# Optimization experiments

Measured on AMD Instinct MI355X. Metric: run time of the kernel, lower is better.

The kernel has to match this reference:

```python
import jax, jax.numpy as jnp
import numpy as np
from jax import lax

NPOINT = 1024
K = 32
EPS = 1e-5  # BatchNorm eps (eval mode, running stats)


def _fps(xyz, npoint):
    """Farthest point sampling. xyz: [B,N,3] -> idx [B,npoint] (int32).
    Deterministic start at index 0 (torch version starts at a random index)."""
    B, N, _ = xyz.shape
    barange = jnp.arange(B)

    def step(carry, _):
        distance, farthest = carry
        centroid = xyz[barange, farthest]                    # [B,3]
        d = jnp.sum((xyz - centroid[:, None, :]) ** 2, -1)   # [B,N]
        distance = jnp.minimum(distance, d)
        new_far = jnp.argmax(distance, axis=-1).astype(jnp.int32)
        return (distance, new_far), farthest

    init = (jnp.full((B, N), 1e10, dtype=xyz.dtype), jnp.zeros((B,), jnp.int32))
    _, centroids = lax.scan(step, init, None, length=npoint)  # [npoint,B]
    return centroids.T                                        # [B,npoint]


def _square_distance(src, dst):
    # src [B,M,3], dst [B,N,3] -> [B,M,N]
    return (jnp.sum(src ** 2, -1)[:, :, None]
            - 2.0 * jnp.einsum('bmc,bnc->bmn', src, dst)
            + jnp.sum(dst ** 2, -1)[:, None, :])


def _gather(p, idx):
    # p [B,N,C], idx [B,...] -> [B,...,C]
    return jax.vmap(lambda pb, ib: pb[ib])(p, idx)


def _mlp_layer(x, w, cb, g, b, m, v):
    # x [B,S,K,Cin]; Conv2d 1x1 == channel matmul, then eval-mode BN, ReLU
    x = jnp.einsum('bskc,oc->bsko', x, w) + cb
    x = (x - m) * (g / jnp.sqrt(v + EPS)) + b
    return jax.nn.relu(x)


def _forward(xyz, points, w0, cb0, g0, b0, m0, v0,
             w1, cb1, g1, b1, m1, v1, w2, cb2, g2, b2, m2, v2):
    fps_idx = _fps(xyz, NPOINT)                       # [B,S]
    new_xyz = _gather(xyz, fps_idx)                   # [B,S,3]
    dists = _square_distance(new_xyz, xyz)            # [B,S,N]
    _, nn_idx = lax.top_k(-dists, K)                  # [B,S,K]
    grouped_xyz = _gather(xyz, nn_idx)                # [B,S,K,3]
    grouped_xyz_norm = grouped_xyz - new_xyz[:, :, None, :]
    grouped_pts = _gather(points, nn_idx)             # [B,S,K,C]
    x = jnp.concatenate([grouped_xyz_norm, grouped_pts], axis=-1)  # [B,S,K,3+C]
    x = _mlp_layer(x, w0, cb0, g0, b0, m0, v0)
    x = _mlp_layer(x, w1, cb1, g1, b1, m1, v1)
    x = _mlp_layer(x, w2, cb2, g2, b2, m2, v2)
    new_points = jnp.max(x, axis=2)                   # max over K -> [B,S,Cout]
    return new_xyz, jnp.transpose(new_points, (0, 2, 1))  # [B,Cout,S]


def setup_inputs() -> dict:
    key = jax.random.key(0)
    ks = jax.random.split(key, 8)
    B, N, C = 16, 4096, 64
    inp = {
        'xyz': jax.random.normal(ks[0], (B, N, 3), jnp.float32),
        'points': jax.random.normal(ks[1], (B, N, C), jnp.float32),
    }
    channels = [(3 + C, 64), (64, 64), (64, 128)]
    for li, (ci, co) in enumerate(channels):
        inp[f'w{li}'] = jax.random.normal(ks[2 + li], (co, ci), jnp.float32) * 0.05
        inp[f'cb{li}'] = jnp.zeros((co,), jnp.float32)
        inp[f'g{li}'] = jnp.ones((co,), jnp.float32)
        inp[f'b{li}'] = jnp.zeros((co,), jnp.float32)
        inp[f'm{li}'] = jnp.zeros((co,), jnp.float32)
        inp[f'v{li}'] = jnp.ones((co,), jnp.float32)
    return inp


def reference(xyz, points, w0, cb0, g0, b0, m0, v0,
              w1, cb1, g1, b1, m1, v1, w2, cb2, g2, b2, m2, v2):
    return _forward(xyz, points, w0, cb0, g0, b0, m0, v0,
                    w1, cb1, g1, b1, m1, v1, w2, cb2, g2, b2, m2, v2)
```

## Files before the change

kernel.cpp:

```cpp
#include <hip/hip_runtime.h>
#include <math.h>

#define NPTS 4096
#define NB 16
#define NS 1024
#define KNB 32
#define CPTS 64

#define FLAG_OFF_B  0
#define CNT_OFF_B   64
#define PUBC_OFF_B  128
#define WFRAG_ELEMS 18432
#define NUNITS      16384
#define CAP         256

typedef __attribute__((ext_vector_type(8))) short short8;
typedef __attribute__((ext_vector_type(4))) float f32x4;

__device__ __forceinline__ short f2bf(float f) {
  unsigned u = __float_as_uint(f);
  unsigned r = (u + 0x7fffu + ((u >> 16) & 1u)) >> 16;
  return (short)r;
}

template <int CTRL>
__device__ __forceinline__ int dppmov(int cur) {
  return __builtin_amdgcn_update_dpp(cur, cur, CTRL, 0xF, 0xF, false);
}
template <int CTRL>
__device__ __forceinline__ void dpp_max_u64(unsigned& hi, unsigned& lo) {
  unsigned nhi = (unsigned)dppmov<CTRL>((int)hi);
  unsigned nlo = (unsigned)dppmov<CTRL>((int)lo);
  bool gt = (nhi > hi) || (nhi == hi && nlo > lo);
  hi = gt ? nhi : hi;
  lo = gt ? nlo : lo;
}
template <int CTRL>
__device__ __forceinline__ void dpp_fmax(float& m) {
  m = fmaxf(m, __int_as_float(dppmov<CTRL>(__float_as_int(m))));
}
template <int CTRL>
__device__ __forceinline__ void dpp_umin(unsigned& v) {
  unsigned o = (unsigned)dppmov<CTRL>((int)v);
  v = (o < v) ? o : v;
}

#define XSTR 104
__global__ __launch_bounds__(512, 2) void fused_kernel(
    const float* __restrict__ xyz, const float* __restrict__ points,
    const float* __restrict__ w0, const float* __restrict__ cb0, const float* __restrict__ g0,
    const float* __restrict__ b0, const float* __restrict__ m0, const float* __restrict__ v0,
    const float* __restrict__ w1, const float* __restrict__ cb1, const float* __restrict__ g1,
    const float* __restrict__ b1, const float* __restrict__ m1, const float* __restrict__ v1,
    const float* __restrict__ w2, const float* __restrict__ cb2, const float* __restrict__ g2,
    const float* __restrict__ b2, const float* __restrict__ m2, const float* __restrict__ v2,
    char* __restrict__ wsb, float* __restrict__ newxyz, float* __restrict__ outp) {
  struct FpsSh {
    float4 sxyz4[NPTS];
    float4 centL[NS];
    unsigned long long part[2][8];
  };
  struct WorkerSh {
    short Wlds[WFRAG_ELEMS];
    short X[8][32 * XSTR];
    unsigned long long cand[8][CAP];
    int nnL[8][KNB];
    float biasL[256];
    unsigned cnt[8];
  };
  __shared__ union { FpsSh f; WorkerSh w; } sh;

  const int t = threadIdx.x;
  const int lane = t & 63;
  const int wave = t >> 6;
  unsigned* flagp = (unsigned*)(wsb + FLAG_OFF_B);
  unsigned* cntp  = (unsigned*)(wsb + CNT_OFF_B);
  float* pubC = (float*)(wsb + PUBC_OFF_B);

  if (blockIdx.x < NB) {
    const int b = blockIdx.x;
    const float* xb = xyz + (size_t)b * NPTS * 3;
    float* outb = newxyz + (size_t)b * NS * 3;

    for (int i = t; i < NPTS; i += 512)
      sh.f.sxyz4[i] = make_float4(xb[i * 3 + 0], xb[i * 3 + 1], xb[i * 3 + 2], 0.f);

    float px[8], py[8], pz[8], dist[8];
#pragma unroll
    for (int j = 0; j < 8; ++j) {
      int n = t + 512 * j;
      px[j] = xb[n * 3 + 0];
      py[j] = xb[n * 3 + 1];
      pz[j] = xb[n * 3 + 2];
      dist[j] = 1e10f;
    }
    __syncthreads();
    float cx = sh.f.sxyz4[0].x, cy = sh.f.sxyz4[0].y, cz = sh.f.sxyz4[0].z;
    if (t == 0) sh.f.centL[0] = sh.f.sxyz4[0];

    for (int it = 1; it < NS; ++it) {
      const int buf = it & 1;
      float dm[8];
#pragma unroll
      for (int j = 0; j < 8; ++j) {
        float dx = __fsub_rn(px[j], cx);
        float dy = __fsub_rn(py[j], cy);
        float dz = __fsub_rn(pz[j], cz);
        float d  = __fadd_rn(__fadd_rn(__fmul_rn(dx, dx), __fmul_rn(dy, dy)), __fmul_rn(dz, dz));
        float v  = fminf(dist[j], d);
        dist[j] = v;
        dm[j] = v;
      }
      float m = fmaxf(fmaxf(fmaxf(dm[0], dm[1]), fmaxf(dm[2], dm[3])),
                      fmaxf(fmaxf(dm[4], dm[5]), fmaxf(dm[6], dm[7])));
      dpp_fmax<0xB1>(m);  dpp_fmax<0x4E>(m);  dpp_fmax<0x141>(m);
      dpp_fmax<0x140>(m); dpp_fmax<0x142>(m); dpp_fmax<0x143>(m);
      float M = __int_as_float(__builtin_amdgcn_readlane(__float_as_int(m), 63));
      unsigned idxl = 0xFFFFFFFFu;
#pragma unroll
      for (int j = 7; j >= 0; --j) idxl = (dm[j] == M) ? (unsigned)(t + 512 * j) : idxl;
      dpp_umin<0xB1>(idxl);  dpp_umin<0x4E>(idxl);  dpp_umin<0x141>(idxl);
      dpp_umin<0x140>(idxl); dpp_umin<0x142>(idxl); dpp_umin<0x143>(idxl);
      if (lane == 63)
        sh.f.part[buf][wave] = ((unsigned long long)__float_as_uint(M) << 32) | (unsigned)(~idxl);
      __syncthreads();
      unsigned long long k0 = sh.f.part[buf][lane & 7];
      unsigned khi = (unsigned)(k0 >> 32), klo = (unsigned)k0;
      dpp_max_u64<0xB1>(khi, klo);
      dpp_max_u64<0x4E>(khi, klo);
      dpp_max_u64<0x141>(khi, klo);
      int bi = (int)(~klo) & 4095;
      float4 c4 = sh.f.sxyz4[bi];
      cx = c4.x; cy = c4.y; cz = c4.z;
      if (t == 0) sh.f.centL[it] = c4;
      if ((it & 31) == 31 && wave == 0) {
        if (lane == 0)
          __hip_atomic_store(&flagp[b], (unsigned)(it - 31), __ATOMIC_RELEASE, __HIP_MEMORY_SCOPE_AGENT);
        if (lane < 32) {
          int ci = it - 31 + lane;
          float4 cc = sh.f.centL[ci];
          float* dst = pubC + ((size_t)b * NS + ci) * 3;
          __hip_atomic_store(dst + 0, cc.x, __ATOMIC_RELAXED, __HIP_MEMORY_SCOPE_AGENT);
          __hip_atomic_store(dst + 1, cc.y, __ATOMIC_RELAXED, __HIP_MEMORY_SCOPE_AGENT);
          __hip_atomic_store(dst + 2, cc.z, __ATOMIC_RELAXED, __HIP_MEMORY_SCOPE_AGENT);
        }
      }
    }
    if (wave == 0 && lane == 0)
      __hip_atomic_store(&flagp[b], (unsigned)NS, __ATOMIC_RELEASE, __HIP_MEMORY_SCOPE_AGENT);
    __syncthreads();
    const float* cf = (const float*)sh.f.centL;
    for (int i = t; i < NS * 3; i += 512) {
      int p = i / 3, c = i - p * 3;
      outb[i] = cf[p * 4 + c];
    }
  }

  __syncthreads();
  for (int i = t; i < WFRAG_ELEMS; i += 512) {
    int g = i >> 9, ln = (i >> 3) & 63, j = i & 7;
    int l, nt, s;
    if (g < 12)      { l = 0; nt = g / 3;  s = g % 3; }
    else if (g < 20) { l = 1; int gg = g - 12; nt = gg >> 1; s = gg & 1; }
    else             { l = 2; int gg = g - 20; nt = gg >> 1; s = gg & 1; }
    int n = nt * 16 + (ln & 15);
    int k = s * 32 + ((ln >> 4) << 3) + j;
    float val = 0.f;
    if (l == 0) { if (k < 67) val = w0[n * 67 + k] * (g0[n] / sqrtf(v0[n] + 1e-5f)); }
    else if (l == 1) { val = w1[n * 64 + k] * (g1[n] / sqrtf(v1[n] + 1e-5f)); }
    else { val = w2[n * 64 + k] * (g2[n] / sqrtf(v2[n] + 1e-5f)); }
    sh.w.Wlds[i] = f2bf(val);
  }
  if (t < 256) {
    int o = t;
    float bv;
    if (o < 64)       { float sc = g0[o] / sqrtf(v0[o] + 1e-5f); bv = (cb0[o] - m0[o]) * sc + b0[o]; }
    else if (o < 128) { int c = o - 64;  float sc = g1[c] / sqrtf(v1[c] + 1e-5f); bv = (cb1[c] - m1[c]) * sc + b1[c]; }
    else              { int c = o - 128; float sc = g2[c] / sqrtf(v2[c] + 1e-5f); bv = (cb2[c] - m2[c]) * sc + b2[c]; }
    sh.w.biasL[o] = bv;
  }
  __syncthreads();

  unsigned long long* cand = sh.w.cand[wave];

  for (;;) {
    unsigned u = 0;
    if (lane == 0) u = atomicAdd(cntp, 1u);
    u = (unsigned)__builtin_amdgcn_readfirstlane((int)u);
    if (u >= NUNITS) break;
    const int b = (int)(u & 15u);
    const int s = (int)(u >> 4);

    {
      unsigned need = (unsigned)s + 1u;
      while (__hip_atomic_load(&flagp[b], __ATOMIC_ACQUIRE, __HIP_MEMORY_SCOPE_AGENT) < need)
        __builtin_amdgcn_s_sleep(64);
    }
    const float* qcp = pubC + ((size_t)b * NS + s) * 3;
    float qx = __hip_atomic_load(qcp + 0, __ATOMIC_RELAXED, __HIP_MEMORY_SCOPE_AGENT);
    float qy = __hip_atomic_load(qcp + 1, __ATOMIC_RELAXED, __HIP_MEMORY_SCOPE_AGENT);
    float qz = __hip_atomic_load(qcp + 2, __ATOMIC_RELAXED, __HIP_MEMORY_SCOPE_AGENT);

    const float* xb = xyz + (size_t)b * NPTS * 3;
    float s2 = __fadd_rn(__fadd_rn(__fmul_rn(qx, qx), __fmul_rn(qy, qy)), __fmul_rn(qz, qz));

    unsigned long long mkey = 0xFFFFFFFFFFFFFFFFull;
#pragma unroll 4
    for (int j = 0; j < 64; ++j) {
      int n = j * 64 + lane;
      float px = xb[n * 3], py = xb[n * 3 + 1], pz = xb[n * 3 + 2];
      float n2 = __fadd_rn(__fadd_rn(__fmul_rn(px, px), __fmul_rn(py, py)), __fmul_rn(pz, pz));
      float dt = __fadd_rn(__fadd_rn(__fmul_rn(qx, px), __fmul_rn(qy, py)), __fmul_rn(qz, pz));
      float d  = __fadd_rn(__fsub_rn(s2, __fmul_rn(2.0f, dt)), n2);
      unsigned uu = __float_as_uint(d);
      uu ^= (0x80000000u | (unsigned)((int)uu >> 31));
      unsigned long long key = ((unsigned long long)uu << 32) | (unsigned)n;
      mkey = key < mkey ? key : mkey;
    }

    {
      unsigned mh = (unsigned)(mkey >> 32), ml2 = (unsigned)mkey;
#pragma unroll
      for (int k = 2; k <= 64; k <<= 1) {
#pragma unroll
        for (int j = k >> 1; j >= 1; j >>= 1) {
          unsigned oh = (unsigned)__shfl_xor((int)mh, j, 64);
          unsigned ol = (unsigned)__shfl_xor((int)ml2, j, 64);
          bool up = (lane & k) == 0;
          bool lower = (lane & j) == 0;
          bool omin = (oh < mh) || (oh == mh && ol < ml2);
          bool keep_o = (lower == up) ? omin : !omin;
          mh = keep_o ? oh : mh;
          ml2 = keep_o ? ol : ml2;
        }
      }
      unsigned th = (unsigned)__builtin_amdgcn_readlane((int)mh, 31);
      unsigned tl = (unsigned)__builtin_amdgcn_readlane((int)ml2, 31);
      mkey = ((unsigned long long)th << 32) | tl;
    }
    const unsigned long long tau = mkey;

    if (lane == 0) sh.w.cnt[wave] = 0;
    asm volatile("s_waitcnt lgkmcnt(0)" ::: "memory");
#pragma unroll 4
    for (int j = 0; j < 64; ++j) {
      int n = j * 64 + lane;
      float px = xb[n * 3], py = xb[n * 3 + 1], pz = xb[n * 3 + 2];
      float n2 = __fadd_rn(__fadd_rn(__fmul_rn(px, px), __fmul_rn(py, py)), __fmul_rn(pz, pz));
      float dt = __fadd_rn(__fadd_rn(__fmul_rn(qx, px), __fmul_rn(qy, py)), __fmul_rn(qz, pz));
      float d  = __fadd_rn(__fsub_rn(s2, __fmul_rn(2.0f, dt)), n2);
      unsigned uu = __float_as_uint(d);
      uu ^= (0x80000000u | (unsigned)((int)uu >> 31));
      unsigned long long key = ((unsigned long long)uu << 32) | (unsigned)n;
      if (key <= tau) {
        unsigned pos = atomicAdd(&sh.w.cnt[wave], 1u);
        if (pos < CAP) cand[pos] = key;
      }
    }
    asm volatile("s_waitcnt lgkmcnt(0)" ::: "memory");
    unsigned cn = sh.w.cnt[wave];
    if (cn > CAP) cn = CAP;

    for (unsigned base = 0; base < cn; base += 64) {
      unsigned i = base + (unsigned)lane;
      unsigned long long ki = (i < cn) ? cand[i] : 0xFFFFFFFFFFFFFFFFull;
      int rank = 0;
#pragma unroll 4
      for (unsigned c2 = 0; c2 < cn; ++c2)
        rank += (cand[c2] < ki) ? 1 : 0;
      if (i < cn && rank < KNB) sh.w.nnL[wave][rank] = (int)(unsigned)(ki & 0xFFFFFFFFull);
    }
    asm volatile("s_waitcnt lgkmcnt(0)" ::: "memory");

    {
      const int qi = wave;
      const float* pb = points + (size_t)b * NPTS * CPTS;
      const float* bias = sh.w.biasL;
      short* X = sh.w.X[qi];

      {
        int r = lane & 31, half = lane >> 5;
        int idx = sh.w.nnL[qi][r];
        const float* prow = pb + (size_t)idx * CPTS;
#pragma unroll
        for (int i = 0; i < 48; ++i) {
          int c = half * 48 + i;
          float v;
          if (c < 3) {
            float qc = (c == 0) ? qx : ((c == 1) ? qy : qz);
            v = __fsub_rn(xb[idx * 3 + c], qc);
          } else if (c < 67) {
            v = prow[c - 3];
          } else {
            v = 0.f;
          }
          X[r * XSTR + c] = f2bf(v);
        }
      }

      const int ml = lane & 15, quad = lane >> 4;
      const short8* Wf = (const short8*)sh.w.Wlds;

      short8 a0[2][3];
#pragma unroll
      for (int m2 = 0; m2 < 2; ++m2)
#pragma unroll
        for (int s3 = 0; s3 < 3; ++s3)
          a0[m2][s3] = *(const short8*)&X[(m2 * 16 + ml) * XSTR + s3 * 32 + quad * 8];
      f32x4 acc0[2][4];
#pragma unroll
      for (int m2 = 0; m2 < 2; ++m2)
#pragma unroll
        for (int nt = 0; nt < 4; ++nt) {
          f32x4 c = {0.f, 0.f, 0.f, 0.f};
#pragma unroll
          for (int s3 = 0; s3 < 3; ++s3)
            c = __builtin_amdgcn_mfma_f32_16x16x32_bf16(a0[m2][s3], Wf[(nt * 3 + s3) * 64 + lane], c, 0, 0, 0);
          acc0[m2][nt] = c;
        }
#pragma unroll
      for (int m2 = 0; m2 < 2; ++m2)
#pragma unroll
        for (int nt = 0; nt < 4; ++nt) {
          int ch = nt * 16 + ml;
          float bv = bias[ch];
#pragma unroll
          for (int r4 = 0; r4 < 4; ++r4) {
            float y = fmaxf(acc0[m2][nt][r4] + bv, 0.f);
            int m = quad * 4 + r4;
            int sK = ch >> 5, qq = (ch >> 3) & 3, jj = ch & 7;
            X[((m2 * 2 + sK) * 64 + qq * 16 + m) * 8 + jj] = f2bf(y);
          }
        }

      short8 a1[2][2];
#pragma unroll
      for (int m2 = 0; m2 < 2; ++m2)
#pragma unroll
        for (int sK = 0; sK < 2; ++sK)
          a1[m2][sK] = *(const short8*)&X[((m2 * 2 + sK) * 64 + lane) * 8];
      f32x4 acc1[2][4];
#pragma unroll
      for (int m2 = 0; m2 < 2; ++m2)
#pragma unroll
        for (int nt = 0; nt < 4; ++nt) {
          f32x4 c = {0.f, 0.f, 0.f, 0.f};
#pragma unroll
          for (int sK = 0; sK < 2; ++sK)
            c = __builtin_amdgcn_mfma_f32_16x16x32_bf16(a1[m2][sK], Wf[(12 + nt * 2 + sK) * 64 + lane], c, 0, 0, 0);
          acc1[m2][nt] = c;
        }
#pragma unroll
      for (int m2 = 0; m2 < 2; ++m2)
#pragma unroll
        for (int nt = 0; nt < 4; ++nt) {
          int ch = nt * 16 + ml;
          float bv = bias[64 + ch];
#pragma unroll
          for (int r4 = 0; r4 < 4; ++r4) {
            float y = fmaxf(acc1[m2][nt][r4] + bv, 0.f);
            int m = quad * 4 + r4;
            int sK = ch >> 5, qq = (ch >> 3) & 3, jj = ch & 7;
            X[((m2 * 2 + sK) * 64 + qq * 16 + m) * 8 + jj] = f2bf(y);
          }
        }

      short8 a2[2][2];
#pragma unroll
      for (int m2 = 0; m2 < 2; ++m2)
#pragma unroll
        for (int sK = 0; sK < 2; ++sK)
          a2[m2][sK] = *(const short8*)&X[((m2 * 2 + sK) * 64 + lane) * 8];
#pragma unroll
      for (int nt = 0; nt < 8; ++nt) {
        f32x4 c0 = {0.f, 0.f, 0.f, 0.f}, c1 = {0.f, 0.f, 0.f, 0.f};
        short8 w0f = Wf[(20 + nt * 2 + 0) * 64 + lane];
        short8 w1f = Wf[(20 + nt * 2 + 1) * 64 + lane];
        c0 = __builtin_amdgcn_mfma_f32_16x16x32_bf16(a2[0][0], w0f, c0, 0, 0, 0);
        c0 = __builtin_amdgcn_mfma_f32_16x16x32_bf16(a2[0][1], w1f, c0, 0, 0, 0);
        c1 = __builtin_amdgcn_mfma_f32_16x16x32_bf16(a2[1][0], w0f, c1, 0, 0, 0);
        c1 = __builtin_amdgcn_mfma_f32_16x16x32_bf16(a2[1][1], w1f, c1, 0, 0, 0);
        float bv = bias[128 + nt * 16 + ml];
        float m = -1.f;
#pragma unroll
        for (int r4 = 0; r4 < 4; ++r4) {
          m = fmaxf(m, fmaxf(c0[r4] + bv, 0.f));
          m = fmaxf(m, fmaxf(c1[r4] + bv, 0.f));
        }
        m = fmaxf(m, __shfl_xor(m, 16, 64));
        m = fmaxf(m, __shfl_xor(m, 32, 64));
        if (lane < 16) outp[((size_t)b * 128 + nt * 16 + lane) * NS + s] = m;
      }
    }
  }
}

extern "C" void kernel_launch(void* const* d_in, const int* in_sizes, int n_in,
                              void* d_out, int out_size, void* d_ws, size_t ws_size,
                              hipStream_t stream) {
  const float* xyz    = (const float*)d_in[0];
  const float* points = (const float*)d_in[1];
  const float* w0  = (const float*)d_in[2];
  const float* cb0 = (const float*)d_in[3];
  const float* g0  = (const float*)d_in[4];
  const float* b0  = (const float*)d_in[5];
  const float* m0  = (const float*)d_in[6];
  const float* v0  = (const float*)d_in[7];
  const float* w1  = (const float*)d_in[8];
  const float* cb1 = (const float*)d_in[9];
  const float* g1  = (const float*)d_in[10];
  const float* b1  = (const float*)d_in[11];
  const float* m1  = (const float*)d_in[12];
  const float* v1  = (const float*)d_in[13];
  const float* w2  = (const float*)d_in[14];
  const float* cb2 = (const float*)d_in[15];
  const float* g2  = (const float*)d_in[16];
  const float* b2  = (const float*)d_in[17];
  const float* m2  = (const float*)d_in[18];
  const float* v2  = (const float*)d_in[19];

  char*  wsb    = (char*)d_ws;
  float* newxyz = (float*)d_out;
  float* outp   = (float*)d_out + (size_t)NB * NS * 3;

  hipMemsetAsync(wsb, 0, 128, stream);
  fused_kernel<<<256, 512, 0, stream>>>(
      xyz, points, w0, cb0, g0, b0, m0, v0, w1, cb1, g1, b1, m1, v1,
      w2, cb2, g2, b2, m2, v2, wsb, newxyz, outp);
}
```

Measured before the change: 955.3 us.

## Batch work grabs, cache FPS flags, vectorize gather, reorder layer-0 channels

Workers now claim 8 units per atomic and keep a per-batch cache of the last seen FPS progress flag in a lane register, so they poll the global flag less often. The FPS publisher swaps its release stores for an explicit vmcnt wait plus a relaxed store, and the per-lane argmax index reduction becomes a tree instead of a serial chain. The neighbor feature gather is rewritten to use float4 loads and short8 LDS stores. To allow this, layer-0 weights are permuted so the 64 point features come first and the 3 xyz offsets sit at columns 64-66, with X zero-filled once up front. The weaker acquire semantics on the flag and pubC loads carry a memory-ordering risk.

```diff
diff --git a/kernel.cpp b/kernel.cpp
--- a/kernel.cpp
+++ b/kernel.cpp
@@ -13,6 +13,7 @@
 #define WFRAG_ELEMS 18432
 #define NUNITS      16384
 #define CAP         256
+#define GRAB        8
 
 typedef __attribute__((ext_vector_type(8))) short short8;
 typedef __attribute__((ext_vector_type(4))) float f32x4;
@@ -116,9 +117,18 @@
       dpp_fmax<0xB1>(m);  dpp_fmax<0x4E>(m);  dpp_fmax<0x141>(m);
       dpp_fmax<0x140>(m); dpp_fmax<0x142>(m); dpp_fmax<0x143>(m);
       float M = __int_as_float(__builtin_amdgcn_readlane(__float_as_int(m), 63));
-      unsigned idxl = 0xFFFFFFFFu;
-#pragma unroll
-      for (int j = 7; j >= 0; --j) idxl = (dm[j] == M) ? (unsigned)(t + 512 * j) : idxl;
+      unsigned i0 = (dm[0] == M) ? (unsigned)(t + 512 * 0) : 0xFFFFFFFFu;
+      unsigned i1 = (dm[1] == M) ? (unsigned)(t + 512 * 1) : 0xFFFFFFFFu;
+      unsigned i2 = (dm[2] == M) ? (unsigned)(t + 512 * 2) : 0xFFFFFFFFu;
+      unsigned i3 = (dm[3] == M) ? (unsigned)(t + 512 * 3) : 0xFFFFFFFFu;
+      unsigned i4 = (dm[4] == M) ? (unsigned)(t + 512 * 4) : 0xFFFFFFFFu;
+      unsigned i5 = (dm[5] == M) ? (unsigned)(t + 512 * 5) : 0xFFFFFFFFu;
+      unsigned i6 = (dm[6] == M) ? (unsigned)(t + 512 * 6) : 0xFFFFFFFFu;
+      unsigned i7 = (dm[7] == M) ? (unsigned)(t + 512 * 7) : 0xFFFFFFFFu;
+      unsigned a01 = i0 < i1 ? i0 : i1, a23 = i2 < i3 ? i2 : i3;
+      unsigned a45 = i4 < i5 ? i4 : i5, a67 = i6 < i7 ? i6 : i7;
+      unsigned a03 = a01 < a23 ? a01 : a23, a47 = a45 < a67 ? a45 : a67;
+      unsigned idxl = a03 < a47 ? a03 : a47;
       dpp_umin<0xB1>(idxl);  dpp_umin<0x4E>(idxl);  dpp_umin<0x141>(idxl);
       dpp_umin<0x140>(idxl); dpp_umin<0x142>(idxl); dpp_umin<0x143>(idxl);
       if (lane == 63)
@@ -134,8 +144,10 @@
       cx = c4.x; cy = c4.y; cz = c4.z;
       if (t == 0) sh.f.centL[it] = c4;
       if ((it & 31) == 31 && wave == 0) {
-        if (lane == 0)
-          __hip_atomic_store(&flagp[b], (unsigned)(it - 31), __ATOMIC_RELEASE, __HIP_MEMORY_SCOPE_AGENT);
+        if (lane == 0) {
+          asm volatile("s_waitcnt vmcnt(0)" ::: "memory");
+          __hip_atomic_store(&flagp[b], (unsigned)(it - 31), __ATOMIC_RELAXED, __HIP_MEMORY_SCOPE_AGENT);
+        }
         if (lane < 32) {
           int ci = it - 31 + lane;
           float4 cc = sh.f.centL[ci];
@@ -146,8 +158,10 @@
         }
       }
     }
-    if (wave == 0 && lane == 0)
-      __hip_atomic_store(&flagp[b], (unsigned)NS, __ATOMIC_RELEASE, __HIP_MEMORY_SCOPE_AGENT);
+    if (wave == 0 && lane == 0) {
+      asm volatile("s_waitcnt vmcnt(0)" ::: "memory");
+      __hip_atomic_store(&flagp[b], (unsigned)NS, __ATOMIC_RELAXED, __HIP_MEMORY_SCOPE_AGENT);
+    }
     __syncthreads();
     const float* cf = (const float*)sh.f.centL;
     for (int i = t; i < NS * 3; i += 512) {
@@ -166,7 +180,11 @@
     int n = nt * 16 + (ln & 15);
     int k = s * 32 + ((ln >> 4) << 3) + j;
     float val = 0.f;
-    if (l == 0) { if (k < 67) val = w0[n * 67 + k] * (g0[n] / sqrtf(v0[n] + 1e-5f)); }
+    if (l == 0) {
+      float sc = g0[n] / sqrtf(v0[n] + 1e-5f);
+      if (k < 64)      val = w0[n * 67 + (k + 3)] * sc;
+      else if (k < 67) val = w0[n * 67 + (k - 64)] * sc;
+    }
     else if (l == 1) { val = w1[n * 64 + k] * (g1[n] / sqrtf(v1[n] + 1e-5f)); }
     else { val = w2[n * 64 + k] * (g2[n] / sqrtf(v2[n] + 1e-5f)); }
     sh.w.Wlds[i] = f2bf(val);
@@ -182,19 +200,35 @@
   __syncthreads();
 
   unsigned long long* cand = sh.w.cand[wave];
+  for (int i = lane; i < (32 * XSTR) / 2; i += 64) ((int*)sh.w.X[wave])[i] = 0;
+
+  unsigned fcache = 0;
 
   for (;;) {
-    unsigned u = 0;
-    if (lane == 0) u = atomicAdd(cntp, 1u);
-    u = (unsigned)__builtin_amdgcn_readfirstlane((int)u);
-    if (u >= NUNITS) break;
+    unsigned base = 0;
+    if (lane == 0) base = atomicAdd(cntp, (unsigned)GRAB);
+    base = (unsigned)__builtin_amdgcn_readfirstlane((int)base);
+    if (base >= NUNITS) break;
+    unsigned uend = base + GRAB;
+    if (uend > NUNITS) uend = NUNITS;
+
+    for (unsigned u = base; u < uend; ++u) {
     const int b = (int)(u & 15u);
     const int s = (int)(u >> 4);
 
     {
       unsigned need = (unsigned)s + 1u;
-      while (__hip_atomic_load(&flagp[b], __ATOMIC_ACQUIRE, __HIP_MEMORY_SCOPE_AGENT) < need)
-        __builtin_amdgcn_s_sleep(64);
+      unsigned have = (unsigned)__shfl((int)fcache, b, 64);
+      if (have < need) {
+        unsigned f;
+        for (;;) {
+          f = __hip_atomic_load(&flagp[b], __ATOMIC_RELAXED, __HIP_MEMORY_SCOPE_AGENT);
+          if (f >= need) break;
+          __builtin_amdgcn_s_sleep(64);
+        }
+        if (lane == b) fcache = f;
+        asm volatile("" ::: "memory");
+      }
     }
     const float* qcp = pubC + ((size_t)b * NS + s) * 3;
     float qx = __hip_atomic_load(qcp + 0, __ATOMIC_RELAXED, __HIP_MEMORY_SCOPE_AGENT);
@@ -261,8 +295,8 @@
     unsigned cn = sh.w.cnt[wave];
     if (cn > CAP) cn = CAP;
 
-    for (unsigned base = 0; base < cn; base += 64) {
-      unsigned i = base + (unsigned)lane;
+    for (unsigned bb = 0; bb < cn; bb += 64) {
+      unsigned i = bb + (unsigned)lane;
       unsigned long long ki = (i < cn) ? cand[i] : 0xFFFFFFFFFFFFFFFFull;
       int rank = 0;
 #pragma unroll 4
@@ -279,23 +313,24 @@
       short* X = sh.w.X[qi];
 
       {
-        int r = lane & 31, half = lane >> 5;
+        int h = lane & 1, r = lane >> 1;
         int idx = sh.w.nnL[qi][r];
-        const float* prow = pb + (size_t)idx * CPTS;
-#pragma unroll
-        for (int i = 0; i < 48; ++i) {
-          int c = half * 48 + i;
-          float v;
-          if (c < 3) {
-            float qc = (c == 0) ? qx : ((c == 1) ? qy : qz);
-            v = __fsub_rn(xb[idx * 3 + c], qc);
-          } else if (c < 67) {
-            v = prow[c - 3];
-          } else {
-            v = 0.f;
-          }
-          X[r * XSTR + c] = f2bf(v);
-        }
+        const f32x4* src = (const f32x4*)(pb + (size_t)idx * CPTS) + h * 8;
+        short8* dst = (short8*)&X[r * XSTR + h * 32];
+#pragma unroll
+        for (int q = 0; q < 4; ++q) {
+          f32x4 v0 = src[q * 2], v1 = src[q * 2 + 1];
+          short8 o;
+          o[0] = f2bf(v0[0]); o[1] = f2bf(v0[1]); o[2] = f2bf(v0[2]); o[3] = f2bf(v0[3]);
+          o[4] = f2bf(v1[0]); o[5] = f2bf(v1[1]); o[6] = f2bf(v1[2]); o[7] = f2bf(v1[3]);
+          dst[q] = o;
+        }
+      }
+      if (lane < 32) {
+        int idx = sh.w.nnL[qi][lane];
+        X[lane * XSTR + 64] = f2bf(__fsub_rn(xb[idx * 3 + 0], qx));
+        X[lane * XSTR + 65] = f2bf(__fsub_rn(xb[idx * 3 + 1], qy));
+        X[lane * XSTR + 66] = f2bf(__fsub_rn(xb[idx * 3 + 2], qz));
       }
 
       const int ml = lane & 15, quad = lane >> 4;
@@ -391,6 +426,7 @@
         m = fmaxf(m, __shfl_xor(m, 32, 64));
         if (lane < 16) outp[((size_t)b * 128 + nt * 16 + lane) * NS + s] = m;
       }
+    }
     }
   }
 }
```

New measurement: 1.028 ms. 7.6% more time.
